# Performance work log

Measured on AMD Instinct MI355X. Metric: run time of the kernel, lower is better.

The kernel has to match this reference:

```python
import jax, jax.numpy as jnp
import numpy as np

EMBD = 1024
HEADS = 16


def setup_inputs() -> dict:
    key = jax.random.key(0)
    ks = jax.random.split(key, 9)
    s = 1.0 / np.sqrt(EMBD)
    X = jax.random.normal(ks[0], (4, 2048, EMBD), dtype=jnp.float32)
    Wq = jax.random.uniform(ks[1], (EMBD, EMBD), jnp.float32, -s, s)
    bq = jax.random.uniform(ks[2], (EMBD,), jnp.float32, -s, s)
    Wk = jax.random.uniform(ks[3], (EMBD, EMBD), jnp.float32, -s, s)
    bk = jax.random.uniform(ks[4], (EMBD,), jnp.float32, -s, s)
    Wv = jax.random.uniform(ks[5], (EMBD, EMBD), jnp.float32, -s, s)
    bv = jax.random.uniform(ks[6], (EMBD,), jnp.float32, -s, s)
    Wo = jax.random.uniform(ks[7], (EMBD, EMBD), jnp.float32, -s, s)
    bo = jax.random.uniform(ks[8], (EMBD,), jnp.float32, -s, s)
    return {"X": X, "Wq": Wq, "bq": bq, "Wk": Wk, "bk": bk,
            "Wv": Wv, "bv": bv, "Wo": Wo, "bo": bo}


def _split_heads(x):
    # [b, n, (h d)] -> [b, h, n, d]
    b, n, e = x.shape
    return x.reshape(b, n, HEADS, e // HEADS).transpose(0, 2, 1, 3)


def reference(X, Wq, bq, Wk, bk, Wv, bv, Wo, bo):
    q = _split_heads(X @ Wq.T + bq)
    k = _split_heads(X @ Wk.T + bk)
    v = _split_heads(X @ Wv.T + bv)
    # NOTE: original scales by sqrt(embdSize), not sqrt(d_head)
    scaling = EMBD ** 0.5
    energy = jnp.einsum('bhqd,bhkd->bhqk', q, k)
    att = jax.nn.softmax(energy / scaling, axis=-1)
    out = jnp.einsum('bhal,bhlv->bhav', att, v)
    b, h, n, d = out.shape
    out = out.transpose(0, 2, 1, 3).reshape(b, n, h * d)
    return out @ Wo.T + bo
```

## Files before the change

### kernel.cpp

```cpp
#include <hip/hip_runtime.h>
#include <hip/hip_bf16.h>

#define EMBD 1024
#define HEADS 16
#define DH 64
#define SEQ 2048
#define NBATCH 4
#define TOK (NBATCH*SEQ)

typedef __hip_bfloat16 bf16;
typedef __bf16 bf16x8 __attribute__((ext_vector_type(8)));
typedef float f32x4 __attribute__((ext_vector_type(4)));
typedef float f32x16 __attribute__((ext_vector_type(16)));
typedef unsigned u32x4 __attribute__((ext_vector_type(4)));

__device__ int g_isf32;
__device__ unsigned short g_Xb[TOK*EMBD];
__device__ unsigned short g_Wb[4][EMBD*EMBD];
__device__ unsigned short g_Q[TOK*EMBD];
__device__ unsigned short g_K[TOK*EMBD];
__device__ unsigned short g_Vt[TOK*EMBD];
__device__ unsigned short g_O[TOK*EMBD];

__device__ __forceinline__ f32x4 mfma16(bf16x8 a, bf16x8 b, f32x4 c) {
    return __builtin_amdgcn_mfma_f32_16x16x32_bf16(a, b, c, 0, 0, 0);
}
__device__ __forceinline__ f32x16 mfma32(bf16x8 a, bf16x8 b, f32x16 c) {
    return __builtin_amdgcn_mfma_f32_32x32x16_bf16(a, b, c, 0, 0, 0);
}

#define GLL16(gp, lp) __builtin_amdgcn_global_load_lds( \
    (__attribute__((address_space(1))) void*)(gp), \
    (__attribute__((address_space(3))) void*)(lp), 16, 0, 0)

#define WAITV8 asm volatile("s_waitcnt vmcnt(8)" ::: "memory")
#define WAITV4 asm volatile("s_waitcnt vmcnt(4)" ::: "memory")
#define WAITV0 asm volatile("s_waitcnt vmcnt(0)" ::: "memory")
#define SBAR   asm volatile("s_barrier" ::: "memory")

__global__ void detect_dtype(const unsigned short* __restrict__ Xu) {
    __shared__ int cnt;
    if (threadIdx.x == 0) cnt = 0;
    __syncthreads();
    int local = 0;
    for (int i = threadIdx.x; i < 1024; i += 256) {
        const unsigned e = (Xu[2*i] >> 7) & 0xFF;
        if (e >= 0x68 && e <= 0x86) local++;
    }
    atomicAdd(&cnt, local);
    __syncthreads();
    if (threadIdx.x == 0) g_isf32 = (cnt < 512) ? 1 : 0;
}

__global__ void __launch_bounds__(256) cvt_all(
    const void* __restrict__ X, const void* __restrict__ Wq,
    const void* __restrict__ Wk, const void* __restrict__ Wv,
    const void* __restrict__ Wo)
{
    const int NV_X = TOK*EMBD/8;
    const int NV_W = EMBD*EMBD/8;
    const long v = (long)blockIdx.x * 256 + threadIdx.x;
    const void* src; unsigned short* dst; long o;
    if (v < NV_X) { src = X; dst = g_Xb; o = v; }
    else {
        const long u = v - NV_X;
        const int wi = (int)(u >> 17);
        o = u & (NV_W - 1);
        src = (wi==0) ? Wq : (wi==1) ? Wk : (wi==2) ? Wv : Wo;
        dst = g_Wb[wi];
    }
    if (g_isf32) {
        const float4* sp = reinterpret_cast<const float4*>(src) + o*2;
        const float4 a = sp[0], b4 = sp[1];
        const float f[8] = {a.x, a.y, a.z, a.w, b4.x, b4.y, b4.z, b4.w};
        unsigned short r[8];
        #pragma unroll
        for (int i = 0; i < 8; ++i) {
            bf16 h = __float2bfloat16(f[i]);
            r[i] = *reinterpret_cast<unsigned short*>(&h);
        }
        *reinterpret_cast<uint4*>(dst + o*8) = *reinterpret_cast<const uint4*>(r);
    } else {
        *reinterpret_cast<uint4*>(dst + o*8) = reinterpret_cast<const uint4*>(src)[o];
    }
}

__global__ void __launch_bounds__(256) qkv_gemm(
    const void* __restrict__ bq, const void* __restrict__ bk,
    const void* __restrict__ bv)
{
    const int z = blockIdx.z;
    const bf16* W    = reinterpret_cast<const bf16*>(g_Wb[z]);
    const void* bias = (z == 0) ? bq : (z == 1) ? bk : bv;
    const bf16* Xb   = reinterpret_cast<const bf16*>(g_Xb);
    const int  isf32 = g_isf32;

    const int tile_m = blockIdx.x * 128;
    const int tile_n = blockIdx.y * 128;
    const int tid  = threadIdx.x;
    const int lane = tid & 63;
    const int w    = tid >> 6;
    const int wr   = w >> 1, wc = w & 1;
    const int g    = lane >> 4, c = lane & 15;
    const int xr   = c >> 1;

    __shared__ __align__(16) bf16 As[2][128*64];
    __shared__ __align__(16) bf16 Bs[2][128*64];

    const bf16* Ab = Xb + tile_m*EMBD;
    const bf16* Bb = W  + tile_n*EMBD;

    f32x4 acc[4][4] = {};

    auto stage = [&](int b, int kt) {
        const int kk = kt*64;
        #pragma unroll
        for (int i = 0; i < 4; ++i) {
            const int li  = i*256 + tid;
            const int row = li >> 3;
            const int cs  = ((li & 7) ^ ((li >> 4) & 7)) << 3;
            GLL16(Ab + row*EMBD + kk + cs, As[b] + li*8);
            GLL16(Bb + row*EMBD + kk + cs, Bs[b] + li*8);
        }
    };

    auto compute = [&](int b) {
        #pragma unroll
        for (int kh = 0; kh < 2; ++kh) {
            const int co = (((kh*4 + g) ^ xr) << 3);
            bf16x8 a[4], bfr[4];
            #pragma unroll
            for (int m = 0; m < 4; ++m)
                a[m] = *reinterpret_cast<const bf16x8*>(
                    As[b] + (wr*64 + m*16 + c)*64 + co);
            #pragma unroll
            for (int n = 0; n < 4; ++n)
                bfr[n] = *reinterpret_cast<const bf16x8*>(
                    Bs[b] + (wc*64 + n*16 + c)*64 + co);
            #pragma unroll
            for (int m = 0; m < 4; ++m)
                #pragma unroll
                for (int n = 0; n < 4; ++n)
                    acc[m][n] = mfma16(a[m], bfr[n], acc[m][n]);
        }
    };

    stage(0, 0);
    stage(1, 1);

    int buf = 0;
    for (int kt = 0; kt < 15; ++kt) {
        WAITV8;
        SBAR;
        compute(buf);
        SBAR;
        if (kt + 2 < 16) stage(buf, kt + 2);
        buf ^= 1;
    }
    WAITV0;
    SBAR;
    compute(buf);

    const float scale = (z == 0) ? 0.04508422f : 1.0f;
    bf16* Qp = reinterpret_cast<bf16*>(g_Q);
    bf16* Kp = reinterpret_cast<bf16*>(g_K);
    bf16* Vp = reinterpret_cast<bf16*>(g_Vt);

    #pragma unroll
    for (int n = 0; n < 4; ++n) {
        const int col = tile_n + wc*64 + n*16 + c;
        const float bval = isf32 ? reinterpret_cast<const float*>(bias)[col]
                                 : __bfloat162float(reinterpret_cast<const bf16*>(bias)[col]);
        const int h = col >> 6, d = col & 63;
        #pragma unroll
        for (int m = 0; m < 4; ++m) {
            const int row0 = tile_m + wr*64 + m*16 + g*4;
            #pragma unroll
            for (int r = 0; r < 4; ++r) {
                const int row = row0 + r;
                const int bb = row >> 11, nn = row & (SEQ-1);
                const bf16 val = __float2bfloat16((acc[m][n][r] + bval) * scale);
                if (z == 0)      Qp[((bb*HEADS + h)*SEQ + nn)*DH + d] = val;
                else if (z == 1) Kp[((bb*HEADS + h)*SEQ + nn)*DH + d] = val;
                else             Vp[((bb*HEADS + h)*DH + d)*SEQ + nn] = val;
            }
        }
    }
}

__device__ __forceinline__ unsigned pk2(float lo, float hi) {
    unsigned r;
    asm("v_cvt_pk_bf16_f32 %0, %1, %2" : "=v"(r) : "v"(lo), "v"(hi));
    return r;
}

__global__ void __launch_bounds__(256, 4) attn_kernel()
{
    const int n   = blockIdx.x;
    const int xcd = n & 7, j = n >> 3;
    const int bh  = xcd*8 + (j >> 4);
    const int qt  = j & 15;
    const int tid = threadIdx.x, lane = tid & 63, wv = tid >> 6;
    const int ql = lane & 31, hi = lane >> 5;
    const int q0 = qt*128 + wv*32;

    const bf16* Qh = reinterpret_cast<const bf16*>(g_Q)  + bh*SEQ*DH;
    const bf16* Kh = reinterpret_cast<const bf16*>(g_K)  + bh*SEQ*DH;
    const bf16* Vh = reinterpret_cast<const bf16*>(g_Vt) + bh*DH*SEQ;
    bf16*       Oh = reinterpret_cast<bf16*>(g_O)        + bh*SEQ*DH;

    __shared__ __align__(16) bf16 Ks[2][4096];
    __shared__ __align__(16) bf16 Vs[2][4096];

    bf16x8 qf[4];
    #pragma unroll
    for (int sd = 0; sd < 4; ++sd)
        qf[sd] = *reinterpret_cast<const bf16x8*>(Qh + (q0 + ql)*DH + sd*16 + hi*8);

    f32x16 minit;
    #pragma unroll
    for (int r = 0; r < 16; ++r) minit[r] = -16.0f;

    const u32x4 onesw = {0x3F803F80u, 0x3F803F80u, 0x3F803F80u, 0x3F803F80u};
    const bf16x8 ones = __builtin_bit_cast(bf16x8, onesw);

    f32x16 oacc[2] = {};
    f32x16 lsacc = {};

    auto stage = [&](int b, int kt) {
        #pragma unroll
        for (int i = 0; i < 2; ++i) {
            const int slot = wv*2 + i;
            const int mt = slot >> 2, sd = slot & 3;
            GLL16(Kh + (kt + 32*mt + ql)*DH + sd*16 + hi*8,
                  Ks[b] + slot*512 + lane*8);
            GLL16(Vh + (32*mt + ql)*SEQ + kt + sd*16 + hi*8,
                  Vs[b] + slot*512 + lane*8);
        }
    };

    stage(0, 0);
    stage(1, 64);

    const int NT = SEQ/64;
    int buf = 0;
    for (int t = 0; t < NT; ++t) {
        if (t < NT - 1) { WAITV4; } else { WAITV0; }
        SBAR;

        #pragma unroll
        for (int st = 0; st < 2; ++st) {
            f32x16 s = minit;
            __builtin_amdgcn_s_setprio(1);
            #pragma unroll
            for (int sd = 0; sd < 4; ++sd) {
                bf16x8 kf = *reinterpret_cast<const bf16x8*>(
                    Ks[buf] + (st*4 + sd)*512 + lane*8);
                s = mfma32(kf, qf[sd], s);
            }
            __builtin_amdgcn_s_setprio(0);

            #pragma unroll
            for (int r = 0; r < 16; ++r) s[r] = __builtin_amdgcn_exp2f(s[r]);

            bf16x8 pb[2];
            #pragma unroll
            for (int jj = 0; jj < 2; ++jj) {
                const int b0 = jj*2, b1 = jj*2 + 1;
                unsigned x0 = pk2(s[4*b0+0], s[4*b0+1]);
                unsigned y0 = pk2(s[4*b1+0], s[4*b1+1]);
                asm("v_permlane32_swap_b32 %0, %1" : "+v"(x0), "+v"(y0));
                unsigned x1 = pk2(s[4*b0+2], s[4*b0+3]);
                unsigned y1 = pk2(s[4*b1+2], s[4*b1+3]);
                asm("v_permlane32_swap_b32 %0, %1" : "+v"(x1), "+v"(y1));
                u32x4 wvec = {x0, x1, y0, y1};
                pb[jj] = __builtin_bit_cast(bf16x8, wvec);
            }

            __builtin_amdgcn_s_setprio(1);
            #pragma unroll
            for (int mt = 0; mt < 2; ++mt)
                #pragma unroll
                for (int jj = 0; jj < 2; ++jj) {
                    bf16x8 vf = *reinterpret_cast<const bf16x8*>(
                        Vs[buf] + (mt*4 + st*2 + jj)*512 + lane*8);
                    oacc[mt] = mfma32(vf, pb[jj], oacc[mt]);
                }
            lsacc = mfma32(ones, pb[0], lsacc);
            lsacc = mfma32(ones, pb[1], lsacc);
            __builtin_amdgcn_s_setprio(0);
        }

        SBAR;
        if (t + 2 < NT) stage(buf, (t + 2)*64);
        buf ^= 1;
    }

    const float inv = 1.0f / lsacc[0];
    #pragma unroll
    for (int mt = 0; mt < 2; ++mt) {
        #pragma unroll
        for (int b = 0; b < 4; ++b) {
            const int d0 = 32*mt + 8*b + 4*hi;
            unsigned short r4[4];
            #pragma unroll
            for (int t = 0; t < 4; ++t) {
                bf16 h = __float2bfloat16(oacc[mt][4*b + t] * inv);
                r4[t] = *reinterpret_cast<unsigned short*>(&h);
            }
            *reinterpret_cast<ushort4*>(Oh + (q0 + ql)*DH + d0) =
                *reinterpret_cast<const ushort4*>(r4);
        }
    }
}

__global__ void __launch_bounds__(256) out_gemm(
    const void* __restrict__ bo, void* __restrict__ Out)
{
    const bf16* Oin = reinterpret_cast<const bf16*>(g_O);
    const bf16* Wo  = reinterpret_cast<const bf16*>(g_Wb[3]);
    const int isf32 = g_isf32;

    const int tile_m = blockIdx.x * 128;
    const int tile_n = blockIdx.y * 128;
    const int tid  = threadIdx.x;
    const int lane = tid & 63;
    const int w    = tid >> 6;
    const int wr   = w >> 1, wc = w & 1;
    const int g    = lane >> 4, c = lane & 15;
    const int xr   = c >> 1;

    __shared__ __align__(16) bf16 As[2][128*64];
    __shared__ __align__(16) bf16 Bs[2][128*64];

    const bf16* Bb = Wo + tile_n*EMBD;

    f32x4 acc[4][4] = {};

    auto stage = [&](int b, int kt) {
        const bf16* Ab = Oin + ((((unsigned)tile_m >> 11)*HEADS + kt)*SEQ
                                + (tile_m & (SEQ-1)))*DH;
        const int kk = kt*64;
        #pragma unroll
        for (int i = 0; i < 4; ++i) {
            const int li  = i*256 + tid;
            const int row = li >> 3;
            const int cs  = ((li & 7) ^ ((li >> 4) & 7)) << 3;
            GLL16(Ab + row*64 + cs, As[b] + li*8);
            GLL16(Bb + row*EMBD + kk + cs, Bs[b] + li*8);
        }
    };

    auto compute = [&](int b) {
        #pragma unroll
        for (int kh = 0; kh < 2; ++kh) {
            const int co = (((kh*4 + g) ^ xr) << 3);
            bf16x8 a[4], bfr[4];
            #pragma unroll
            for (int m = 0; m < 4; ++m)
                a[m] = *reinterpret_cast<const bf16x8*>(
                    As[b] + (wr*64 + m*16 + c)*64 + co);
            #pragma unroll
            for (int n = 0; n < 4; ++n)
                bfr[n] = *reinterpret_cast<const bf16x8*>(
                    Bs[b] + (wc*64 + n*16 + c)*64 + co);
            #pragma unroll
            for (int m = 0; m < 4; ++m)
                #pragma unroll
                for (int n = 0; n < 4; ++n)
                    acc[m][n] = mfma16(a[m], bfr[n], acc[m][n]);
        }
    };

    stage(0, 0);
    stage(1, 1);

    int buf = 0;
    for (int kt = 0; kt < 15; ++kt) {
        WAITV8;
        SBAR;
        compute(buf);
        SBAR;
        if (kt + 2 < 16) stage(buf, kt + 2);
        buf ^= 1;
    }
    WAITV0;
    SBAR;
    compute(buf);

    #pragma unroll
    for (int n = 0; n < 4; ++n) {
        const int col = tile_n + wc*64 + n*16 + c;
        const float bval = isf32 ? reinterpret_cast<const float*>(bo)[col]
                                 : __bfloat162float(reinterpret_cast<const bf16*>(bo)[col]);
        #pragma unroll
        for (int m = 0; m < 4; ++m) {
            const int row0 = tile_m + wr*64 + m*16 + g*4;
            #pragma unroll
            for (int r = 0; r < 4; ++r) {
                const float val = acc[m][n][r] + bval;
                const int idx = (row0 + r)*EMBD + col;
                if (isf32) reinterpret_cast<float*>(Out)[idx] = val;
                else       reinterpret_cast<bf16*>(Out)[idx] = __float2bfloat16(val);
            }
        }
    }
}

extern "C" void kernel_launch(void* const* d_in, const int* in_sizes, int n_in,
                              void* d_out, int out_size, void* d_ws, size_t ws_size,
                              hipStream_t stream) {
    (void)in_sizes; (void)n_in; (void)out_size; (void)d_ws; (void)ws_size;
    const void* X  = d_in[0];
    const void* Wq = d_in[1];
    const void* bq = d_in[2];
    const void* Wk = d_in[3];
    const void* bk = d_in[4];
    const void* Wv = d_in[5];
    const void* bv = d_in[6];
    const void* Wo = d_in[7];
    const void* bo = d_in[8];

    detect_dtype<<<dim3(1), dim3(256), 0, stream>>>((const unsigned short*)X);
    cvt_all<<<dim3((TOK*EMBD/8 + 4*EMBD*EMBD/8)/256), dim3(256), 0, stream>>>(X, Wq, Wk, Wv, Wo);
    qkv_gemm<<<dim3(TOK/128, EMBD/128, 3), dim3(256), 0, stream>>>(bq, bk, bv);
    attn_kernel<<<dim3(16*NBATCH*HEADS), dim3(256), 0, stream>>>();
    out_gemm<<<dim3(TOK/128, EMBD/128), dim3(256), 0, stream>>>(bo, d_out);
}
```

Baseline: 205.6 us.

## Switch projection GEMMs to triple-buffered K=32 tiles

```diff
diff --git a/kernel.cpp b/kernel.cpp
--- a/kernel.cpp
+++ b/kernel.cpp
@@ -102,10 +102,10 @@
     const int w    = tid >> 6;
     const int wr   = w >> 1, wc = w & 1;
     const int g    = lane >> 4, c = lane & 15;
-    const int xr   = c >> 1;
-
-    __shared__ __align__(16) bf16 As[2][128*64];
-    __shared__ __align__(16) bf16 Bs[2][128*64];
+    const int xr   = (c >> 1) & 3;
+
+    __shared__ __align__(16) bf16 As[3][128*32];
+    __shared__ __align__(16) bf16 Bs[3][128*32];
 
     const bf16* Ab = Xb + tile_m*EMBD;
     const bf16* Bb = W  + tile_n*EMBD;
@@ -113,53 +113,51 @@
     f32x4 acc[4][4] = {};
 
     auto stage = [&](int b, int kt) {
-        const int kk = kt*64;
-        #pragma unroll
-        for (int i = 0; i < 4; ++i) {
+        const int kk = kt*32;
+        #pragma unroll
+        for (int i = 0; i < 2; ++i) {
             const int li  = i*256 + tid;
-            const int row = li >> 3;
-            const int cs  = ((li & 7) ^ ((li >> 4) & 7)) << 3;
+            const int row = li >> 2;
+            const int cs  = (((li & 3) ^ ((li >> 3) & 3)) << 3);
             GLL16(Ab + row*EMBD + kk + cs, As[b] + li*8);
             GLL16(Bb + row*EMBD + kk + cs, Bs[b] + li*8);
         }
     };
 
     auto compute = [&](int b) {
-        #pragma unroll
-        for (int kh = 0; kh < 2; ++kh) {
-            const int co = (((kh*4 + g) ^ xr) << 3);
-            bf16x8 a[4], bfr[4];
-            #pragma unroll
-            for (int m = 0; m < 4; ++m)
-                a[m] = *reinterpret_cast<const bf16x8*>(
-                    As[b] + (wr*64 + m*16 + c)*64 + co);
+        const int co = ((g ^ xr) << 3);
+        bf16x8 a[4], bfr[4];
+        #pragma unroll
+        for (int m = 0; m < 4; ++m)
+            a[m] = *reinterpret_cast<const bf16x8*>(
+                As[b] + (wr*64 + m*16 + c)*32 + co);
+        #pragma unroll
+        for (int n = 0; n < 4; ++n)
+            bfr[n] = *reinterpret_cast<const bf16x8*>(
+                Bs[b] + (wc*64 + n*16 + c)*32 + co);
+        #pragma unroll
+        for (int m = 0; m < 4; ++m)
             #pragma unroll
             for (int n = 0; n < 4; ++n)
-                bfr[n] = *reinterpret_cast<const bf16x8*>(
-                    Bs[b] + (wc*64 + n*16 + c)*64 + co);
-            #pragma unroll
-            for (int m = 0; m < 4; ++m)
-                #pragma unroll
-                for (int n = 0; n < 4; ++n)
-                    acc[m][n] = mfma16(a[m], bfr[n], acc[m][n]);
-        }
+                acc[m][n] = mfma16(a[m], bfr[n], acc[m][n]);
     };
 
     stage(0, 0);
     stage(1, 1);
-
+    stage(2, 2);
+
+    const int NKT = EMBD/32;
     int buf = 0;
-    for (int kt = 0; kt < 15; ++kt) {
-        WAITV8;
+    for (int kt = 0; kt < NKT; ++kt) {
+        if (kt < NKT-2)      { WAITV8; }
+        else if (kt == NKT-2){ WAITV4; }
+        else                 { WAITV0; }
         SBAR;
         compute(buf);
         SBAR;
-        if (kt + 2 < 16) stage(buf, kt + 2);
-        buf ^= 1;
-    }
-    WAITV0;
-    SBAR;
-    compute(buf);
+        if (kt + 3 < NKT) stage(buf, kt + 3);
+        buf = (buf == 2) ? 0 : buf + 1;
+    }
 
     const float scale = (z == 0) ? 0.04508422f : 1.0f;
     bf16* Qp = reinterpret_cast<bf16*>(g_Q);
@@ -328,65 +326,63 @@
     const int w    = tid >> 6;
     const int wr   = w >> 1, wc = w & 1;
     const int g    = lane >> 4, c = lane & 15;
-    const int xr   = c >> 1;
-
-    __shared__ __align__(16) bf16 As[2][128*64];
-    __shared__ __align__(16) bf16 Bs[2][128*64];
+    const int xr   = (c >> 1) & 3;
+
+    __shared__ __align__(16) bf16 As[3][128*32];
+    __shared__ __align__(16) bf16 Bs[3][128*32];
 
     const bf16* Bb = Wo + tile_n*EMBD;
 
     f32x4 acc[4][4] = {};
 
     auto stage = [&](int b, int kt) {
-        const bf16* Ab = Oin + ((((unsigned)tile_m >> 11)*HEADS + kt)*SEQ
-                                + (tile_m & (SEQ-1)))*DH;
-        const int kk = kt*64;
-        #pragma unroll
-        for (int i = 0; i < 4; ++i) {
+        const bf16* Ab = Oin + ((((unsigned)tile_m >> 11)*HEADS + (kt >> 1))*SEQ
+                                + (tile_m & (SEQ-1)))*DH + (kt & 1)*32;
+        const int kk = kt*32;
+        #pragma unroll
+        for (int i = 0; i < 2; ++i) {
             const int li  = i*256 + tid;
-            const int row = li >> 3;
-            const int cs  = ((li & 7) ^ ((li >> 4) & 7)) << 3;
-            GLL16(Ab + row*64 + cs, As[b] + li*8);
+            const int row = li >> 2;
+            const int cs  = (((li & 3) ^ ((li >> 3) & 3)) << 3);
+            GLL16(Ab + row*DH + cs, As[b] + li*8);
             GLL16(Bb + row*EMBD + kk + cs, Bs[b] + li*8);
         }
     };
 
     auto compute = [&](int b) {
-        #pragma unroll
-        for (int kh = 0; kh < 2; ++kh) {
-            const int co = (((kh*4 + g) ^ xr) << 3);
-            bf16x8 a[4], bfr[4];
-            #pragma unroll
-            for (int m = 0; m < 4; ++m)
-                a[m] = *reinterpret_cast<const bf16x8*>(
-                    As[b] + (wr*64 + m*16 + c)*64 + co);
+        const int co = ((g ^ xr) << 3);
+        bf16x8 a[4], bfr[4];
+        #pragma unroll
+        for (int m = 0; m < 4; ++m)
+            a[m] = *reinterpret_cast<const bf16x8*>(
+                As[b] + (wr*64 + m*16 + c)*32 + co);
+        #pragma unroll
+        for (int n = 0; n < 4; ++n)
+            bfr[n] = *reinterpret_cast<const bf16x8*>(
+                Bs[b] + (wc*64 + n*16 + c)*32 + co);
+        #pragma unroll
+        for (int m = 0; m < 4; ++m)
             #pragma unroll
             for (int n = 0; n < 4; ++n)
-                bfr[n] = *reinterpret_cast<const bf16x8*>(
-                    Bs[b] + (wc*64 + n*16 + c)*64 + co);
-            #pragma unroll
-            for (int m = 0; m < 4; ++m)
-                #pragma unroll
-                for (int n = 0; n < 4; ++n)
-                    acc[m][n] = mfma16(a[m], bfr[n], acc[m][n]);
-        }
+                acc[m][n] = mfma16(a[m], bfr[n], acc[m][n]);
     };
 
     stage(0, 0);
     stage(1, 1);
-
+    stage(2, 2);
+
+    const int NKT = EMBD/32;
     int buf = 0;
-    for (int kt = 0; kt < 15; ++kt) {
-        WAITV8;
+    for (int kt = 0; kt < NKT; ++kt) {
+        if (kt < NKT-2)      { WAITV8; }
+        else if (kt == NKT-2){ WAITV4; }
+        else                 { WAITV0; }
         SBAR;
         compute(buf);
         SBAR;
-        if (kt + 2 < 16) stage(buf, kt + 2);
-        buf ^= 1;
-    }
-    WAITV0;
-    SBAR;
-    compute(buf);
+        if (kt + 3 < NKT) stage(buf, kt + 3);
+        buf = (buf == 2) ? 0 : buf + 1;
+    }
 
     #pragma unroll
     for (int n = 0; n < 4; ++n) {
```

Measured after the change: 215.0 us. 4.6% more time.
